# Kernel tuning notes

Hardware: AMD Instinct MI355X
Metric: run time of the kernel (lower is better)

The kernel has to match this reference:

```python
import jax, jax.numpy as jnp
import numpy as np

INPUT_DIM = 128
HIDDEN_DIM = 128
WINDOW_SIZE = 256
BLOCK_SIZE = 256
BATCH = 8
SEQ = 8192


def setup_inputs() -> dict:
    key = jax.random.key(0)
    ks = jax.random.split(key, 7)
    s = 1.0 / np.sqrt(INPUT_DIM)
    return {
        "x": jax.random.normal(ks[0], (BATCH, SEQ, INPUT_DIM), dtype=jnp.float32),
        "Wq": jax.random.normal(ks[1], (HIDDEN_DIM, INPUT_DIM), dtype=jnp.float32) * s,
        "bq": jax.random.normal(ks[2], (HIDDEN_DIM,), dtype=jnp.float32) * s,
        "Wk": jax.random.normal(ks[3], (HIDDEN_DIM, INPUT_DIM), dtype=jnp.float32) * s,
        "bk": jax.random.normal(ks[4], (HIDDEN_DIM,), dtype=jnp.float32) * s,
        "Wv": jax.random.normal(ks[5], (HIDDEN_DIM, INPUT_DIM), dtype=jnp.float32) * s,
        "bv": jax.random.normal(ks[6], (HIDDEN_DIM,), dtype=jnp.float32) * s,
    }


def reference(x, Wq, bq, Wk, bk, Wv, bv):
    B, S, D = x.shape
    bs, w = BLOCK_SIZE, WINDOW_SIZE
    nb = S // bs
    halo = w - 1
    W = bs + 2 * halo  # per-block K/V window width

    q = x @ Wq.T + bq  # [B,S,H]
    k = x @ Wk.T + bk
    v = x @ Wv.T + bv

    # Zero-pad K/V by halo on both sides. Since there is NO softmax, padded
    # zero keys give zero scores and padded zero values contribute zero —
    # this exactly reproduces the torch code's clamped window slicing.
    k_pad = jnp.pad(k, ((0, 0), (halo, halo), (0, 0)))
    v_pad = jnp.pad(v, ((0, 0), (halo, halo), (0, 0)))

    # Gather overlapping windows: [B, nb, W, H]
    starts = jnp.arange(nb) * bs  # window start in padded coords
    idx = starts[:, None] + jnp.arange(W)[None, :]  # [nb, W]
    k_win = k_pad[:, idx, :]
    v_win = v_pad[:, idx, :]

    q_blk = q.reshape(B, nb, bs, -1)  # [B, nb, bs, H]

    scale = 1.0 / jnp.sqrt(jnp.float32(D))
    attn = jnp.einsum('bnqh,bnkh->bnqk', q_blk, k_win) * scale  # no softmax
    out = jnp.einsum('bnqk,bnkh->bnqh', attn, v_win)
    return out.reshape(B, S, -1)
```

## Files before the change

### kernel.cpp

```cpp
#include <hip/hip_runtime.h>
#include <stdint.h>


#define B_ 8
#define S_ 8192
#define LDW 136
#define LDT 264

using bf16x8 = __attribute__((ext_vector_type(8))) short;
using s16x4  = __attribute__((ext_vector_type(4))) short;
using f32x16 = __attribute__((ext_vector_type(16))) float;

__device__ __forceinline__ short f2bf(float f) {
  union { float f; uint32_t u; } v; v.f = f;
  uint32_t r = v.u + 0x7fffu + ((v.u >> 16) & 1u);
  return (short)(r >> 16);
}
__device__ __forceinline__ float bf2f(short s) {
  union { uint32_t u; float f; } v; v.u = ((uint32_t)(uint16_t)s) << 16;
  return v.f;
}

__global__ __launch_bounds__(512) void kv_kernel(
    const float* __restrict__ x,
    const float* __restrict__ Wk, const float* __restrict__ bk,
    const float* __restrict__ Wv, const float* __restrict__ bv,
    float* __restrict__ Cpart, short* __restrict__ kedge,
    short* __restrict__ vedge)
{
  __shared__ __align__(16) char smem[135168];
  short* areaA = (short*)smem;
  short* areaB = (short*)(smem + 67584);

  const int tid  = threadIdx.x;
  const int lane = tid & 63;
  const int wv   = tid >> 6;
  const int c    = lane & 31;
  const int hl   = lane >> 5;
  const int wg   = ((int)blockIdx.x & 7) * 32 + ((int)blockIdx.x >> 3);
  const int r0   = wg * 256;
  const int b    = r0 >> 13;
  const int n    = (r0 & (S_ - 1)) >> 8;

  bf16x8 afrag[8];
  {
    const float* xrow = x + (size_t)(r0 + wv * 32 + c) * 128 + hl * 8;
    #pragma unroll
    for (int kst = 0; kst < 8; ++kst) {
      const float4* p = (const float4*)(xrow + kst * 16);
      float4 f0 = p[0], f1 = p[1];
      bf16x8 a;
      a[0] = f2bf(f0.x); a[1] = f2bf(f0.y); a[2] = f2bf(f0.z); a[3] = f2bf(f0.w);
      a[4] = f2bf(f1.x); a[5] = f2bf(f1.y); a[6] = f2bf(f1.z); a[7] = f2bf(f1.w);
      afrag[kst] = a;
    }
  }

  auto stageW = [&](const float* W, short* wl) {
    #pragma unroll
    for (int it = 0; it < 8; ++it) {
      int l  = it * 512 + tid;
      int nn = l >> 5;
      int k4 = (l & 31) << 2;
      const float4 f = *(const float4*)(W + nn * 128 + k4);
      s16x4 o;
      o[0] = f2bf(f.x); o[1] = f2bf(f.y); o[2] = f2bf(f.z); o[3] = f2bf(f.w);
      *(s16x4*)(wl + nn * LDW + k4) = o;
    }
  };

  auto gemm = [&](const float* bias, f32x16* acc, const short* wl) {
    #pragma unroll
    for (int nt = 0; nt < 4; ++nt) {
      float bvv = bias[nt * 32 + c];
      #pragma unroll
      for (int i = 0; i < 16; ++i) acc[nt][i] = bvv;
    }
    #pragma unroll
    for (int kst = 0; kst < 8; ++kst) {
      #pragma unroll
      for (int nt = 0; nt < 4; ++nt) {
        bf16x8 bb = *(const bf16x8*)(wl + (nt * 32 + c) * LDW + kst * 16 + hl * 8);
        acc[nt] = __builtin_amdgcn_mfma_f32_32x32x16_bf16(afrag[kst], bb, acc[nt], 0, 0, 0);
      }
    }
  };

  auto writeTransposedLDS = [&](f32x16* acc, short* wl) {
    #pragma unroll
    for (int nt = 0; nt < 4; ++nt) {
      int d = nt * 32 + c;
      #pragma unroll
      for (int g = 0; g < 4; ++g) {
        #pragma unroll
        for (int p = 0; p < 2; ++p) {
          int reg = g * 4 + p * 2;
          int sl  = wv * 32 + g * 8 + hl * 4 + p * 2;
          uint32_t pk = (uint32_t)(uint16_t)f2bf(acc[nt][reg]) |
                        ((uint32_t)(uint16_t)f2bf(acc[nt][reg + 1]) << 16);
          *(uint32_t*)(wl + d * LDT + sl) = pk;
        }
      }
    }
  };

  stageW(Wk, areaA);
  stageW(Wv, areaB);
  __syncthreads();

  f32x16 kacc[4], vacc[4];
  gemm(bk, kacc, areaA);
  gemm(bv, vacc, areaB);
  __syncthreads();

  writeTransposedLDS(kacc, areaA);
  writeTransposedLDS(vacc, areaB);
  __syncthreads();

  {
    const int ht = wv >> 1;
    const int dh = wv & 1;
    f32x16 cacc[2];
    #pragma unroll
    for (int t = 0; t < 2; ++t)
      #pragma unroll
      for (int i = 0; i < 16; ++i) cacc[t][i] = 0.f;

    #pragma unroll
    for (int kst = 0; kst < 16; ++kst) {
      bf16x8 a  = *(const bf16x8*)(areaB + (ht * 32 + c) * LDT + kst * 16 + hl * 8);
      bf16x8 b0 = *(const bf16x8*)(areaA + (dh * 64 + c) * LDT + kst * 16 + hl * 8);
      bf16x8 b1 = *(const bf16x8*)(areaA + (dh * 64 + 32 + c) * LDT + kst * 16 + hl * 8);
      cacc[0] = __builtin_amdgcn_mfma_f32_32x32x16_bf16(a, b0, cacc[0], 0, 0, 0);
      cacc[1] = __builtin_amdgcn_mfma_f32_32x32x16_bf16(a, b1, cacc[1], 0, 0, 0);
    }

    {
      size_t eo = ((size_t)(b * 32 + n)) * 256;
      if (tid < 128)      kedge[eo + tid]               = areaA[tid * LDT + 0];
      else if (tid < 256) kedge[eo + 128 + (tid - 128)] = areaA[(tid - 128) * LDT + 255];
      else if (tid < 384) vedge[eo + (tid - 256)]       = areaB[(tid - 256) * LDT + 0];
      else                vedge[eo + 128 + (tid - 384)] = areaB[(tid - 384) * LDT + 255];
    }

    float* Cp = Cpart + ((size_t)(b * 32 + n)) * 16384;
    #pragma unroll
    for (int t = 0; t < 2; ++t) {
      #pragma unroll
      for (int reg = 0; reg < 16; ++reg) {
        int row = (reg & 3) + 8 * (reg >> 2) + 4 * hl;
        Cp[(ht * 32 + row) * 128 + dh * 64 + t * 32 + c] = cacc[t][reg];
      }
    }
  }
}

__global__ __launch_bounds__(512) void attn_kernel(
    const float* __restrict__ x,
    const float* __restrict__ Wq, const float* __restrict__ bq,
    const float* __restrict__ Cpart,
    const short* __restrict__ kedge, const short* __restrict__ vedge,
    float* __restrict__ out)
{
  __shared__ __align__(16) char smem[104960];
  short* wqT   = (short*)smem;
  short* m_l   = (short*)(smem + 34816);
  short* n_l   = (short*)(smem + 69632);
  float* bqM_l = (float*)(smem + 104448);
  float* opat  = (float*)smem;

  const int tid  = threadIdx.x;
  const int lane = tid & 63;
  const int wv   = tid >> 6;
  const int c    = lane & 31;
  const int hl   = lane >> 5;
  const int wg   = ((int)blockIdx.x & 7) * 32 + ((int)blockIdx.x >> 3);
  const int r0   = wg * 256;
  const int b    = r0 >> 13;
  const int n    = (r0 & (S_ - 1)) >> 8;

  bf16x8 afrag[8];
  {
    const float* xrow = x + (size_t)(r0 + wv * 32 + c) * 128 + hl * 8;
    #pragma unroll
    for (int kst = 0; kst < 8; ++kst) {
      const float4* p = (const float4*)(xrow + kst * 16);
      float4 f0 = p[0], f1 = p[1];
      bf16x8 a;
      a[0] = f2bf(f0.x); a[1] = f2bf(f0.y); a[2] = f2bf(f0.z); a[3] = f2bf(f0.w);
      a[4] = f2bf(f1.x); a[5] = f2bf(f1.y); a[6] = f2bf(f1.z); a[7] = f2bf(f1.w);
      afrag[kst] = a;
    }
  }

  #pragma unroll
  for (int it = 0; it < 8; ++it) {
    int l  = it * 512 + tid;
    int f  = l >> 5;
    int d4 = (l & 31) << 2;
    const float4 w = *(const float4*)(Wq + f * 128 + d4);
    wqT[(d4 + 0) * LDW + f] = f2bf(w.x);
    wqT[(d4 + 1) * LDW + f] = f2bf(w.y);
    wqT[(d4 + 2) * LDW + f] = f2bf(w.z);
    wqT[(d4 + 3) * LDW + f] = f2bf(w.w);
  }

  float m[32];
  #pragma unroll
  for (int i = 0; i < 32; ++i) m[i] = 0.f;

  const float* Cb0 = Cpart + (size_t)b * 32 * 16384;
  #pragma unroll
  for (int e = 0; e < 3; ++e) {
    int nn = n - 1 + e;
    if (nn < 0 || nn > 31) continue;
    const float4* Cp = (const float4*)(Cb0 + (size_t)nn * 16384);
    #pragma unroll
    for (int i4 = 0; i4 < 8; ++i4) {
      float4 f = Cp[i4 * 512 + tid];
      m[i4 * 4 + 0] += f.x; m[i4 * 4 + 1] += f.y;
      m[i4 * 4 + 2] += f.z; m[i4 * 4 + 3] += f.w;
    }
  }

  const int d0 = (tid & 31) << 2;
  if (n > 0) {
    const short* ke = kedge + ((size_t)(b * 32 + n - 1)) * 256;
    const short* ve = vedge + ((size_t)(b * 32 + n - 1)) * 256;
    float k0 = bf2f(ke[d0]),     k1 = bf2f(ke[d0 + 1]);
    float k2 = bf2f(ke[d0 + 2]), k3 = bf2f(ke[d0 + 3]);
    #pragma unroll
    for (int i4 = 0; i4 < 8; ++i4) {
      float vs = bf2f(ve[i4 * 16 + (tid >> 5)]);
      m[i4 * 4 + 0] -= vs * k0; m[i4 * 4 + 1] -= vs * k1;
      m[i4 * 4 + 2] -= vs * k2; m[i4 * 4 + 3] -= vs * k3;
    }
  }
  if (n < 31) {
    const short* ke = kedge + ((size_t)(b * 32 + n + 1)) * 256 + 128;
    const short* ve = vedge + ((size_t)(b * 32 + n + 1)) * 256 + 128;
    float k0 = bf2f(ke[d0]),     k1 = bf2f(ke[d0 + 1]);
    float k2 = bf2f(ke[d0 + 2]), k3 = bf2f(ke[d0 + 3]);
    #pragma unroll
    for (int i4 = 0; i4 < 8; ++i4) {
      float vs = bf2f(ve[i4 * 16 + (tid >> 5)]);
      m[i4 * 4 + 0] -= vs * k0; m[i4 * 4 + 1] -= vs * k1;
      m[i4 * 4 + 2] -= vs * k2; m[i4 * 4 + 3] -= vs * k3;
    }
  }

  const float scale = 0.08838834764831845f;
  float4 bqv = *(const float4*)(bq + d0);
  float bp[8];
  #pragma unroll
  for (int i4 = 0; i4 < 8; ++i4) {
    int h = i4 * 16 + (tid >> 5);
    float m0 = m[i4 * 4 + 0] * scale, m1 = m[i4 * 4 + 1] * scale;
    float m2 = m[i4 * 4 + 2] * scale, m3 = m[i4 * 4 + 3] * scale;
    s16x4 o;
    o[0] = f2bf(m0); o[1] = f2bf(m1); o[2] = f2bf(m2); o[3] = f2bf(m3);
    *(s16x4*)(m_l + h * LDW + d0) = o;
    bp[i4] = m0 * bqv.x + m1 * bqv.y + m2 * bqv.z + m3 * bqv.w;
  }
  #pragma unroll
  for (int mask = 1; mask <= 16; mask <<= 1) {
    #pragma unroll
    for (int i4 = 0; i4 < 8; ++i4) bp[i4] += __shfl_xor(bp[i4], mask);
  }
  if ((tid & 31) == 0) {
    #pragma unroll
    for (int i4 = 0; i4 < 8; ++i4) bqM_l[i4 * 16 + (tid >> 5)] = bp[i4];
  }
  __syncthreads();

  {
    const int ht2 = wv >> 1;
    const int dc  = (wv & 1) * 64;
    f32x16 nacc[2];
    #pragma unroll
    for (int t = 0; t < 2; ++t)
      #pragma unroll
      for (int i = 0; i < 16; ++i) nacc[t][i] = 0.f;

    #pragma unroll
    for (int kst = 0; kst < 8; ++kst) {
      bf16x8 a = *(const bf16x8*)(m_l + (ht2 * 32 + c) * LDW + kst * 16 + hl * 8);
      #pragma unroll
      for (int t = 0; t < 2; ++t) {
        bf16x8 bb = *(const bf16x8*)(wqT + (dc + t * 32 + c) * LDW + kst * 16 + hl * 8);
        nacc[t] = __builtin_amdgcn_mfma_f32_32x32x16_bf16(a, bb, nacc[t], 0, 0, 0);
      }
    }
    #pragma unroll
    for (int t = 0; t < 2; ++t) {
      #pragma unroll
      for (int reg = 0; reg < 16; ++reg) {
        int row = (reg & 3) + 8 * (reg >> 2) + 4 * hl;
        n_l[(ht2 * 32 + row) * LDW + dc + t * 32 + c] = f2bf(nacc[t][reg]);
      }
    }
  }
  __syncthreads();

  f32x16 oacc[4];
  #pragma unroll
  for (int nt = 0; nt < 4; ++nt)
    #pragma unroll
    for (int i = 0; i < 16; ++i) oacc[nt][i] = 0.f;

  #pragma unroll
  for (int kst = 0; kst < 8; ++kst) {
    #pragma unroll
    for (int nt = 0; nt < 4; ++nt) {
      bf16x8 bb = *(const bf16x8*)(n_l + (nt * 32 + c) * LDW + kst * 16 + hl * 8);
      oacc[nt] = __builtin_amdgcn_mfma_f32_32x32x16_bf16(afrag[kst], bb, oacc[nt], 0, 0, 0);
    }
  }

  float* patch = opat + wv * (32 * 36);
  float* outb  = out + ((size_t)r0 + wv * 32) * 128;
  #pragma unroll
  for (int nt = 0; nt < 4; ++nt) {
    float bias = bqM_l[nt * 32 + c];
    #pragma unroll
    for (int reg = 0; reg < 16; ++reg) {
      int row = (reg & 3) + 8 * (reg >> 2) + 4 * hl;
      patch[row * 36 + c] = oacc[nt][reg] + bias;
    }
    #pragma unroll
    for (int p = 0; p < 4; ++p) {
      int row = p * 8 + (lane >> 3);
      float4 vv = *(const float4*)(patch + row * 36 + (lane & 7) * 4);
      *(float4*)(outb + (size_t)row * 128 + nt * 32 + (lane & 7) * 4) = vv;
    }
  }
}

extern "C" void kernel_launch(void* const* d_in, const int* in_sizes, int n_in,
                              void* d_out, int out_size, void* d_ws, size_t ws_size,
                              hipStream_t stream) {
  const float* x  = (const float*)d_in[0];
  const float* Wq = (const float*)d_in[1];
  const float* bq = (const float*)d_in[2];
  const float* Wk = (const float*)d_in[3];
  const float* bk = (const float*)d_in[4];
  const float* Wv = (const float*)d_in[5];
  const float* bv = (const float*)d_in[6];
  float* out = (float*)d_out;

  float* Cpart = (float*)d_ws;
  short* kedge = (short*)(Cpart + (size_t)8 * 32 * 16384);
  short* vedge = kedge + (size_t)8 * 32 * 256;

  kv_kernel<<<256, 512, 0, stream>>>(x, Wk, bk, Wv, bv, Cpart, kedge, vedge);
  attn_kernel<<<256, 512, 0, stream>>>(x, Wq, bq, Cpart, kedge, vedge, out);
}
```

Measured before the change: 117.1 us.

## Split KV partial-product kernel into half-blocks of 128 rows for more workgroups

The KV kernel now processes 128-row half-blocks with 256 threads, so it launches 512 workgroups instead of 256 and uses about half the LDS per workgroup. This is meant to raise occupancy and spread the work across all CUs. In exchange, the attention kernel must sum six partial K^T·V products per block instead of three, which doubles the Cpart workspace traffic. The edge-row bookkeeping is adjusted to use two slots per block.

```diff
diff --git a/kernel.cpp b/kernel.cpp
--- a/kernel.cpp
+++ b/kernel.cpp
@@ -5,7 +5,6 @@
 #define B_ 8
 #define S_ 8192
 #define LDW 136
-#define LDT 264
 
 using bf16x8 = __attribute__((ext_vector_type(8))) short;
 using s16x4  = __attribute__((ext_vector_type(4))) short;
@@ -21,26 +20,25 @@
   return v.f;
 }
 
-__global__ __launch_bounds__(512) void kv_kernel(
+__global__ __launch_bounds__(256) void kv_kernel(
     const float* __restrict__ x,
     const float* __restrict__ Wk, const float* __restrict__ bk,
     const float* __restrict__ Wv, const float* __restrict__ bv,
     float* __restrict__ Cpart, short* __restrict__ kedge,
     short* __restrict__ vedge)
 {
-  __shared__ __align__(16) char smem[135168];
-  short* areaA = (short*)smem;
-  short* areaB = (short*)(smem + 67584);
+  __shared__ __align__(16) short areaA[128 * LDW];
+  __shared__ __align__(16) short areaB[128 * LDW];
 
   const int tid  = threadIdx.x;
   const int lane = tid & 63;
   const int wv   = tid >> 6;
   const int c    = lane & 31;
   const int hl   = lane >> 5;
-  const int wg   = ((int)blockIdx.x & 7) * 32 + ((int)blockIdx.x >> 3);
-  const int r0   = wg * 256;
+  const int wg   = ((int)blockIdx.x & 7) * 64 + ((int)blockIdx.x >> 3);
+  const int r0   = wg * 128;
   const int b    = r0 >> 13;
-  const int n    = (r0 & (S_ - 1)) >> 8;
+  const int j    = (r0 & (S_ - 1)) >> 7;
 
   bf16x8 afrag[8];
   {
@@ -58,8 +56,8 @@
 
   auto stageW = [&](const float* W, short* wl) {
     #pragma unroll
-    for (int it = 0; it < 8; ++it) {
-      int l  = it * 512 + tid;
+    for (int it = 0; it < 16; ++it) {
+      int l  = it * 256 + tid;
       int nn = l >> 5;
       int k4 = (l & 31) << 2;
       const float4 f = *(const float4*)(W + nn * 128 + k4);
@@ -98,7 +96,7 @@
           int sl  = wv * 32 + g * 8 + hl * 4 + p * 2;
           uint32_t pk = (uint32_t)(uint16_t)f2bf(acc[nt][reg]) |
                         ((uint32_t)(uint16_t)f2bf(acc[nt][reg + 1]) << 16);
-          *(uint32_t*)(wl + d * LDT + sl) = pk;
+          *(uint32_t*)(wl + d * LDW + sl) = pk;
         }
       }
     }
@@ -118,38 +116,37 @@
   __syncthreads();
 
   {
-    const int ht = wv >> 1;
-    const int dh = wv & 1;
-    f32x16 cacc[2];
-    #pragma unroll
-    for (int t = 0; t < 2; ++t)
-      #pragma unroll
-      for (int i = 0; i < 16; ++i) cacc[t][i] = 0.f;
-
-    #pragma unroll
-    for (int kst = 0; kst < 16; ++kst) {
-      bf16x8 a  = *(const bf16x8*)(areaB + (ht * 32 + c) * LDT + kst * 16 + hl * 8);
-      bf16x8 b0 = *(const bf16x8*)(areaA + (dh * 64 + c) * LDT + kst * 16 + hl * 8);
-      bf16x8 b1 = *(const bf16x8*)(areaA + (dh * 64 + 32 + c) * LDT + kst * 16 + hl * 8);
-      cacc[0] = __builtin_amdgcn_mfma_f32_32x32x16_bf16(a, b0, cacc[0], 0, 0, 0);
-      cacc[1] = __builtin_amdgcn_mfma_f32_32x32x16_bf16(a, b1, cacc[1], 0, 0, 0);
+    f32x16 cacc[4];
+    #pragma unroll
+    for (int nt = 0; nt < 4; ++nt)
+      #pragma unroll
+      for (int i = 0; i < 16; ++i) cacc[nt][i] = 0.f;
+
+    #pragma unroll
+    for (int kst = 0; kst < 8; ++kst) {
+      bf16x8 a = *(const bf16x8*)(areaB + (wv * 32 + c) * LDW + kst * 16 + hl * 8);
+      #pragma unroll
+      for (int nt = 0; nt < 4; ++nt) {
+        bf16x8 bb = *(const bf16x8*)(areaA + (nt * 32 + c) * LDW + kst * 16 + hl * 8);
+        cacc[nt] = __builtin_amdgcn_mfma_f32_32x32x16_bf16(a, bb, cacc[nt], 0, 0, 0);
+      }
     }
 
     {
-      size_t eo = ((size_t)(b * 32 + n)) * 256;
-      if (tid < 128)      kedge[eo + tid]               = areaA[tid * LDT + 0];
-      else if (tid < 256) kedge[eo + 128 + (tid - 128)] = areaA[(tid - 128) * LDT + 255];
-      else if (tid < 384) vedge[eo + (tid - 256)]       = areaB[(tid - 256) * LDT + 0];
-      else                vedge[eo + 128 + (tid - 384)] = areaB[(tid - 384) * LDT + 255];
-    }
-
-    float* Cp = Cpart + ((size_t)(b * 32 + n)) * 16384;
-    #pragma unroll
-    for (int t = 0; t < 2; ++t) {
+      const int slot = j & 1;
+      const int col  = slot ? 127 : 0;
+      size_t eo = ((size_t)(b * 32 + (j >> 1))) * 256 + slot * 128;
+      if (tid < 128)      kedge[eo + tid]         = areaA[tid * LDW + col];
+      else                vedge[eo + (tid - 128)] = areaB[(tid - 128) * LDW + col];
+    }
+
+    float* Cp = Cpart + ((size_t)(b * 64 + j)) * 16384;
+    #pragma unroll
+    for (int nt = 0; nt < 4; ++nt) {
       #pragma unroll
       for (int reg = 0; reg < 16; ++reg) {
         int row = (reg & 3) + 8 * (reg >> 2) + 4 * hl;
-        Cp[(ht * 32 + row) * 128 + dh * 64 + t * 32 + c] = cacc[t][reg];
+        Cp[(wv * 32 + row) * 128 + nt * 32 + c] = cacc[nt][reg];
       }
     }
   }
@@ -209,12 +206,12 @@
   #pragma unroll
   for (int i = 0; i < 32; ++i) m[i] = 0.f;
 
-  const float* Cb0 = Cpart + (size_t)b * 32 * 16384;
-  #pragma unroll
-  for (int e = 0; e < 3; ++e) {
-    int nn = n - 1 + e;
-    if (nn < 0 || nn > 31) continue;
-    const float4* Cp = (const float4*)(Cb0 + (size_t)nn * 16384);
+  const float* Cb0 = Cpart + (size_t)b * 64 * 16384;
+  #pragma unroll
+  for (int e = 0; e < 6; ++e) {
+    int hj = 2 * n - 2 + e;
+    if (hj < 0 || hj >= 64) continue;
+    const float4* Cp = (const float4*)(Cb0 + (size_t)hj * 16384);
     #pragma unroll
     for (int i4 = 0; i4 < 8; ++i4) {
       float4 f = Cp[i4 * 512 + tid];
@@ -349,9 +346,9 @@
   float* out = (float*)d_out;
 
   float* Cpart = (float*)d_ws;
-  short* kedge = (short*)(Cpart + (size_t)8 * 32 * 16384);
+  short* kedge = (short*)(Cpart + (size_t)8 * 64 * 16384);
   short* vedge = kedge + (size_t)8 * 32 * 256;
 
-  kv_kernel<<<256, 512, 0, stream>>>(x, Wk, bk, Wv, bv, Cpart, kedge, vedge);
+  kv_kernel<<<512, 256, 0, stream>>>(x, Wk, bk, Wv, bv, Cpart, kedge, vedge);
   attn_kernel<<<256, 512, 0, stream>>>(x, Wq, bq, Cpart, kedge, vedge, out);
 }
```

Result: slower. 131.7 us (+12.4%).
